# Performance work log

Hardware: AMD Instinct MI355X
Metric: run time of the kernel (lower is better)

Reference implementation:

```python
import jax, jax.numpy as jnp
import numpy as np

B, N, E = 4, 10000, 160000
F_IN, D_ATT, H = 64, 128, 8
D_K = D_ATT // H  # 16


def setup_inputs() -> dict:
    key = jax.random.key(0)
    ks = jax.random.split(key, 8)
    x = jax.random.normal(ks[0], (B, N, F_IN), dtype=jnp.float32)
    edge = jax.random.randint(ks[1], (2, E), 0, N, dtype=jnp.int64)
    scale = 0.05
    Qw = jax.random.normal(ks[2], (D_ATT, F_IN), dtype=jnp.float32) * scale
    Qb = jnp.zeros((D_ATT,), dtype=jnp.float32)
    Kw = jax.random.normal(ks[3], (D_ATT, F_IN), dtype=jnp.float32) * scale
    Kb = jnp.zeros((D_ATT,), dtype=jnp.float32)
    Vw = jax.random.normal(ks[4], (D_ATT, F_IN), dtype=jnp.float32) * scale
    Vb = jnp.zeros((D_ATT,), dtype=jnp.float32)
    return {"x": x, "Qw": Qw, "Qb": Qb, "Kw": Kw, "Kb": Kb, "Vw": Vw, "Vb": Vb, "edge": edge}


def _proj(x, W, b):
    # x: (B, N, F_IN) -> (B, N, D_K, H)  (view to (B,N,H,D_K) then transpose(2,3))
    y = jnp.einsum('bnf,af->bna', x, W) + b  # (B, N, D_ATT)
    y = y.reshape(y.shape[0], y.shape[1], H, D_K)
    return jnp.swapaxes(y, 2, 3)  # (B, N, D_K, H)


def reference(x, Qw, Qb, Kw, Kb, Vw, Vb, edge):
    q = _proj(x, Qw, Qb)  # (B, N, D_K, H)
    k = _proj(x, Kw, Kb)
    v = _proj(x, Vw, Vb)
    src = q[:, edge[0], :, :]    # (B, E, D_K, H) gather by source node
    dst_k = k[:, edge[1], :, :]  # (B, E, D_K, H) gather by dest node
    prods = jnp.sum(src * dst_k, axis=2) / np.float32(np.sqrt(D_K))  # (B, E, H)
    attention = jax.nn.softmax(prods, axis=1)  # softmax over the edge dimension, as in original
    return attention, v
```

## Files before the change

kernel.cpp:

```cpp
#include <hip/hip_runtime.h>
#include <hip/hip_bf16.h>

constexpr int B  = 4;
constexpr int N  = 10000;
constexpr int E  = 160000;
constexpr int F  = 64;
constexpr int DA = 128;
constexpr int H  = 8;
constexpr int DK = 16;
constexpr int TOTAL = B * N;

constexpr int EPB  = 256;
constexpr int NBLK = E / EPB;
constexpr int RB   = 64;

typedef __attribute__((ext_vector_type(8))) short short8v;
typedef __attribute__((ext_vector_type(4))) float f32x4;
typedef __attribute__((ext_vector_type(2))) float f32x2;

__device__ __forceinline__ unsigned pack_bf16(float a, float b) {
    unsigned ua = __builtin_bit_cast(unsigned, a);
    unsigned ub = __builtin_bit_cast(unsigned, b);
    ua = (ua + 0x7fffu + ((ua >> 16) & 1u)) >> 16;
    ub = (ub + 0x7fffu + ((ub >> 16) & 1u)) >> 16;
    return ua | (ub << 16);
}
__device__ __forceinline__ short8v cvt8(float4 a, float4 b) {
    union { unsigned u[4]; short8v s; } r;
    r.u[0] = pack_bf16(a.x, a.y);
    r.u[1] = pack_bf16(a.z, a.w);
    r.u[2] = pack_bf16(b.x, b.y);
    r.u[3] = pack_bf16(b.z, b.w);
    return r.s;
}
__device__ __forceinline__ int dot8(unsigned a, unsigned b, int c) {
#if __has_builtin(__builtin_amdgcn_sdot8)
    return __builtin_amdgcn_sdot8((int)a, (int)b, c, false);
#else
    #pragma unroll
    for (int n = 0; n < 8; ++n) {
        int av = ((int)(a << (28 - 4 * n))) >> 28;
        int bv = ((int)(b << (28 - 4 * n))) >> 28;
        c += av * bv;
    }
    return c;
#endif
}

__global__ __launch_bounds__(256) void proj_mfma(
    const float* __restrict__ x,
    const float* __restrict__ Qw, const float* __restrict__ Kw,
    const float* __restrict__ Vw,
    const float* __restrict__ Qb, const float* __restrict__ Kb,
    const float* __restrict__ Vb,
    unsigned char* __restrict__ qws, unsigned char* __restrict__ kws,
    float* __restrict__ vout)
{
    __shared__ unsigned char wlds[DA * F * 2];
    __shared__ unsigned char xlds[64 * 256];

    const int t = threadIdx.x;
    const int w = t >> 6, lane = t & 63;
    const int tn = lane & 15, g = lane >> 4;
    const int m0t = blockIdx.x * 64 + w * 16;
    const int mat = blockIdx.y;

    const float* W    = (mat == 0) ? Qw : (mat == 1) ? Kw : Vw;
    const float* bias = (mat == 0) ? Qb : (mat == 1) ? Kb : Vb;
    const float sc = (mat < 2) ? 4.0f : 1.0f;

    float bv[8];
    if (mat < 2) {
        const int base = (tn >> 1) * 16 + (tn & 1) * 8;
        #pragma unroll
        for (int a0t = 0; a0t < 8; ++a0t) bv[a0t] = bias[base + a0t] * 4.0f;
    } else {
        #pragma unroll
        for (int a0t = 0; a0t < 8; ++a0t) bv[a0t] = bias[a0t * 16 + tn];
    }

    {
        const char* xblk = (const char*)(x + (size_t)blockIdx.x * 64 * F);
        #pragma unroll
        for (int j = 0; j < 4; ++j) {
            const int A = j * 4096 + t * 16;
            float4 v = *(const float4*)(xblk + A);
            *(float4*)(xlds + (A ^ (((A >> 8) & 7) << 4))) = v;
        }
    }

    #pragma unroll
    for (int j = 0; j < 4; ++j) {
        const int A = j * 4096 + t * 16;
        const int rho = A >> 7;
        const int srow = (mat < 2)
            ? (((rho >> 1) & 7) * 16 + (rho & 1) * 8 + (rho >> 4))
            : rho;
        const float4* s4 = (const float4*)(W + srow * 64 + ((A & 127) >> 1));
        float4 v0 = s4[0], v1 = s4[1];
        uint4 v;
        v.x = pack_bf16(v0.x * sc, v0.y * sc);
        v.y = pack_bf16(v0.z * sc, v0.w * sc);
        v.z = pack_bf16(v1.x * sc, v1.y * sc);
        v.w = pack_bf16(v1.z * sc, v1.w * sc);
        *(uint4*)(wlds + (A ^ (((A >> 7) & 7) << 4))) = v;
    }
    __syncthreads();

    const int xrow = w * 16 + tn;
    const int xsw  = (xrow & 7) << 4;
    const int xb   = xrow * 256;
    const float4 x0 = *(const float4*)(xlds + ((xb + g * 32)       ^ xsw));
    const float4 x1 = *(const float4*)(xlds + ((xb + g * 32 + 16)  ^ xsw));
    const float4 x2 = *(const float4*)(xlds + ((xb + 128 + g * 32) ^ xsw));
    const float4 x3 = *(const float4*)(xlds + ((xb + 144 + g * 32) ^ xsw));
    const short8v a0 = cvt8(x0, x1);
    const short8v a1 = cvt8(x2, x3);

    const int sw = (tn & 7) << 4;

    f32x4 acc[8];
    #pragma unroll
    for (int a0t = 0; a0t < 8; ++a0t) {
        acc[a0t][0] = bv[a0t]; acc[a0t][1] = bv[a0t];
        acc[a0t][2] = bv[a0t]; acc[a0t][3] = bv[a0t];
    }
    #pragma unroll
    for (int a0t = 0; a0t < 8; ++a0t) {
        const int rowb = (a0t * 16 + tn) * 128;
        short8v b0 = *(const short8v*)(wlds + ((rowb + g * 16) ^ sw));
        short8v b1 = *(const short8v*)(wlds + ((rowb + 64 + g * 16) ^ sw));
        acc[a0t] = __builtin_amdgcn_mfma_f32_16x16x32_bf16(a0, b0, acc[a0t], 0, 0, 0);
        acc[a0t] = __builtin_amdgcn_mfma_f32_16x16x32_bf16(a1, b1, acc[a0t], 0, 0, 0);
    }

    if (mat < 2) {
        unsigned char* qk_dst = (mat == 0) ? qws : kws;
        #pragma unroll
        for (int r = 0; r < 4; ++r) {
            const int node = m0t + g * 4 + r;
            unsigned nib = 0;
            #pragma unroll
            for (int p = 0; p < 8; ++p) {
                float cl = fminf(fmaxf(acc[p][r], -7.f), 7.f);
                int iv = (int)rintf(cl);
                nib |= ((unsigned)(iv & 0xF)) << (4 * p);
            }
            *(unsigned*)(qk_dst + (size_t)node * RB + tn * 4) = nib;
        }
    } else {
        #pragma unroll
        for (int r = 0; r < 4; ++r) {
            const int node = m0t + g * 4 + r;
            float* vb = vout + (size_t)node * DA + tn * 8;
            *(float4*)vb       = make_float4(acc[0][r], acc[1][r], acc[2][r], acc[3][r]);
            *(float4*)(vb + 4) = make_float4(acc[4][r], acc[5][r], acc[6][r], acc[7][r]);
        }
    }
}

__global__ __launch_bounds__(256) void gather_dot_sm(
    const unsigned char* __restrict__ qws, const unsigned char* __restrict__ kws,
    const int* __restrict__ edge, unsigned short* __restrict__ expws,
    float* __restrict__ psum)
{
    const int b   = blockIdx.x;
    const int blk = blockIdx.y;
    const int t = threadIdx.x;
    const int w = t >> 6, lane = t & 63;
    const int g = lane >> 2, i = lane & 3;

    const unsigned char* qb = qws + (size_t)b * N * RB;
    const unsigned char* kb = kws + (size_t)b * N * RB;
    unsigned short* expb = expws + (size_t)b * E * 4;

    const int ew0 = blk * EPB + w * 64;

    const int i0 = ew0 + lane;
    const int s0p = edge[i0];
    const int d0p = edge[E + i0];

    float sa0 = 0.f, sa1 = 0.f;

    #pragma unroll
    for (int r = 0; r < 4; ++r) {
        const int el = ew0 + r * 16 + g;
        const int srcl = r * 16 + g;
        const int s = __shfl(s0p, srcl);
        const int d = __shfl(d0p, srcl);
        const uint4 q = *((const uint4*)(qb + (size_t)s * RB) + i);
        const uint4 k = *((const uint4*)(kb + (size_t)d * RB) + i);

        int dh0 = dot8(q.x, k.x, 0);  dh0 = dot8(q.y, k.y, dh0);
        int dh1 = dot8(q.z, k.z, 0);  dh1 = dot8(q.w, k.w, dh1);

        const float e0 = __expf((float)dh0 * 0.015625f);
        const float e1 = __expf((float)dh1 * 0.015625f);
        const unsigned pk = (unsigned)__builtin_amdgcn_cvt_pk_fp8_f32(e0, e1, 0, false);
        expb[(size_t)el * 4 + i] = (unsigned short)pk;
        sa0 += e0;
        sa1 += e1;
    }

    #pragma unroll
    for (int off = 4; off <= 32; off <<= 1) {
        sa0 += __shfl_xor(sa0, off);
        sa1 += __shfl_xor(sa1, off);
    }

    __shared__ float2 red[4][4];
    if (g == 0) red[w][i] = make_float2(sa0, sa1);
    __syncthreads();
    if (t < 4) {
        float s0f = 0.f, s1f = 0.f;
        #pragma unroll
        for (int ww = 0; ww < 4; ++ww) {
            float2 v = red[ww][t];
            s0f += v.x;
            s1f += v.y;
        }
        psum[((size_t)b * H + 2 * t)     * NBLK + blk] = s0f;
        psum[((size_t)b * H + 2 * t + 1) * NBLK + blk] = s1f;
    }
}

__global__ __launch_bounds__(256) void softmax_norm(
    const unsigned short* __restrict__ expws, float* __restrict__ att,
    const float* __restrict__ psum)
{
    const int b   = blockIdx.x;
    const int blk = blockIdx.y;
    const int t = threadIdx.x;
    const int w = t >> 6, lane = t & 63;

    __shared__ float inv[H];
    {
        const float* p0 = psum + ((size_t)b * H + 2 * w) * NBLK;
        const float* p1 = psum + ((size_t)b * H + 2 * w + 1) * NBLK;
        float s0 = 0.f, s1 = 0.f;
        for (int c = lane; c < NBLK; c += 64) {
            s0 += p0[c];
            s1 += p1[c];
        }
        #pragma unroll
        for (int off = 1; off < 64; off <<= 1) {
            s0 += __shfl_xor(s0, off);
            s1 += __shfl_xor(s1, off);
        }
        if (lane == 0) {
            inv[2 * w]     = 1.0f / s0;
            inv[2 * w + 1] = 1.0f / s1;
        }
    }
    __syncthreads();

    const int el = blk * EPB + t;
    const uint2 u = ((const uint2*)(expws + (size_t)b * E * 4))[el];
    float* p = att + ((size_t)b * E + el) * H;
    const f32x2 e01 = __builtin_amdgcn_cvt_pk_f32_fp8((int)u.x, false);
    const f32x2 e23 = __builtin_amdgcn_cvt_pk_f32_fp8((int)u.x, true);
    const f32x2 e45 = __builtin_amdgcn_cvt_pk_f32_fp8((int)u.y, false);
    const f32x2 e67 = __builtin_amdgcn_cvt_pk_f32_fp8((int)u.y, true);
    float4 v0, v1;
    v0.x = e01[0] * inv[0];  v0.y = e01[1] * inv[1];
    v0.z = e23[0] * inv[2];  v0.w = e23[1] * inv[3];
    v1.x = e45[0] * inv[4];  v1.y = e45[1] * inv[5];
    v1.z = e67[0] * inv[6];  v1.w = e67[1] * inv[7];
    *(float4*)p       = v0;
    *(float4*)(p + 4) = v1;
}

extern "C" void kernel_launch(void* const* d_in, const int* in_sizes, int n_in,
                              void* d_out, int out_size, void* d_ws, size_t ws_size,
                              hipStream_t stream)
{
    const float* x  = (const float*)d_in[0];
    const float* Qw = (const float*)d_in[1];
    const float* Qb = (const float*)d_in[2];
    const float* Kw = (const float*)d_in[3];
    const float* Kb = (const float*)d_in[4];
    const float* Vw = (const float*)d_in[5];
    const float* Vb = (const float*)d_in[6];
    const int*   edge = (const int*)d_in[7];

    float* out  = (float*)d_out;
    float* att  = out;
    float* vout = out + (size_t)B * E * H;

    char* w = (char*)d_ws;
    unsigned char* qws = (unsigned char*)w;
    unsigned char* kws = qws + (size_t)B * N * RB;
    unsigned short* expws = (unsigned short*)(w + 2 * (size_t)B * N * RB);
    float* psum = (float*)(expws + (size_t)B * E * 4);

    hipLaunchKernelGGL(proj_mfma, dim3(TOTAL / 64, 3), dim3(256), 0, stream,
                       x, Qw, Kw, Vw, Qb, Kb, Vb, qws, kws, vout);
    hipLaunchKernelGGL(gather_dot_sm, dim3(B, NBLK), dim3(256), 0, stream,
                       qws, kws, edge, expws, psum);
    hipLaunchKernelGGL(softmax_norm, dim3(B, NBLK), dim3(256), 0, stream,
                       expws, att, psum);
}
```

Baseline: 39.23 us.

## Fuse Q/K/V projections into one block per row tile, stage V stores via LDS

The projection kernel now computes Q, K and V for the same 64-node tile in one block instead of using a third grid dimension. The x tile is loaded and converted once and reused across all three weight matrices held in a larger LDS buffer. The V output is staged through swizzled LDS so each block writes its 32KB contiguously with coalesced float4 stores. The cost is three times the weight LDS footprint and weight conversion per block, which lowers occupancy and reduces grid parallelism.

```diff
diff --git a/kernel.cpp b/kernel.cpp
--- a/kernel.cpp
+++ b/kernel.cpp
@@ -56,27 +56,23 @@
     unsigned char* __restrict__ qws, unsigned char* __restrict__ kws,
     float* __restrict__ vout)
 {
-    __shared__ unsigned char wlds[DA * F * 2];
+    __shared__ unsigned char wlds[3 * DA * F * 2];
     __shared__ unsigned char xlds[64 * 256];
 
     const int t = threadIdx.x;
     const int w = t >> 6, lane = t & 63;
     const int tn = lane & 15, g = lane >> 4;
     const int m0t = blockIdx.x * 64 + w * 16;
-    const int mat = blockIdx.y;
-
-    const float* W    = (mat == 0) ? Qw : (mat == 1) ? Kw : Vw;
-    const float* bias = (mat == 0) ? Qb : (mat == 1) ? Kb : Vb;
-    const float sc = (mat < 2) ? 4.0f : 1.0f;
-
-    float bv[8];
-    if (mat < 2) {
+
+    float bvq[8], bvk[8], bvv[8];
+    {
         const int base = (tn >> 1) * 16 + (tn & 1) * 8;
         #pragma unroll
-        for (int a0t = 0; a0t < 8; ++a0t) bv[a0t] = bias[base + a0t] * 4.0f;
-    } else {
-        #pragma unroll
-        for (int a0t = 0; a0t < 8; ++a0t) bv[a0t] = bias[a0t * 16 + tn];
+        for (int a0t = 0; a0t < 8; ++a0t) {
+            bvq[a0t] = Qb[base + a0t] * 4.0f;
+            bvk[a0t] = Kb[base + a0t] * 4.0f;
+            bvv[a0t] = Vb[a0t * 16 + tn];
+        }
     }
 
     {
@@ -90,13 +86,16 @@
     }
 
     #pragma unroll
-    for (int j = 0; j < 4; ++j) {
-        const int A = j * 4096 + t * 16;
-        const int rho = A >> 7;
-        const int srow = (mat < 2)
+    for (int j = 0; j < 12; ++j) {
+        const float* W = (j < 4) ? Qw : (j < 8) ? Kw : Vw;
+        const float sc = (j < 8) ? 4.0f : 1.0f;
+        const int A  = j * 4096 + t * 16;
+        const int Al = A & 16383;
+        const int rho = Al >> 7;
+        const int srow = (j < 8)
             ? (((rho >> 1) & 7) * 16 + (rho & 1) * 8 + (rho >> 4))
             : rho;
-        const float4* s4 = (const float4*)(W + srow * 64 + ((A & 127) >> 1));
+        const float4* s4 = (const float4*)(W + srow * 64 + ((Al & 127) >> 1));
         float4 v0 = s4[0], v1 = s4[1];
         uint4 v;
         v.x = pack_bf16(v0.x * sc, v0.y * sc);
@@ -119,22 +118,24 @@
 
     const int sw = (tn & 7) << 4;
 
-    f32x4 acc[8];
-    #pragma unroll
-    for (int a0t = 0; a0t < 8; ++a0t) {
-        acc[a0t][0] = bv[a0t]; acc[a0t][1] = bv[a0t];
-        acc[a0t][2] = bv[a0t]; acc[a0t][3] = bv[a0t];
-    }
-    #pragma unroll
-    for (int a0t = 0; a0t < 8; ++a0t) {
-        const int rowb = (a0t * 16 + tn) * 128;
-        short8v b0 = *(const short8v*)(wlds + ((rowb + g * 16) ^ sw));
-        short8v b1 = *(const short8v*)(wlds + ((rowb + 64 + g * 16) ^ sw));
-        acc[a0t] = __builtin_amdgcn_mfma_f32_16x16x32_bf16(a0, b0, acc[a0t], 0, 0, 0);
-        acc[a0t] = __builtin_amdgcn_mfma_f32_16x16x32_bf16(a1, b1, acc[a0t], 0, 0, 0);
-    }
-
-    if (mat < 2) {
+    #pragma unroll
+    for (int mat = 0; mat < 2; ++mat) {
+        const float* bv = (mat == 0) ? bvq : bvk;
+        const unsigned char* wm = wlds + mat * (DA * F * 2);
+        f32x4 acc[8];
+        #pragma unroll
+        for (int a0t = 0; a0t < 8; ++a0t) {
+            acc[a0t][0] = bv[a0t]; acc[a0t][1] = bv[a0t];
+            acc[a0t][2] = bv[a0t]; acc[a0t][3] = bv[a0t];
+        }
+        #pragma unroll
+        for (int a0t = 0; a0t < 8; ++a0t) {
+            const int rowb = (a0t * 16 + tn) * 128;
+            short8v b0 = *(const short8v*)(wm + ((rowb + g * 16) ^ sw));
+            short8v b1 = *(const short8v*)(wm + ((rowb + 64 + g * 16) ^ sw));
+            acc[a0t] = __builtin_amdgcn_mfma_f32_16x16x32_bf16(a0, b0, acc[a0t], 0, 0, 0);
+            acc[a0t] = __builtin_amdgcn_mfma_f32_16x16x32_bf16(a1, b1, acc[a0t], 0, 0, 0);
+        }
         unsigned char* qk_dst = (mat == 0) ? qws : kws;
         #pragma unroll
         for (int r = 0; r < 4; ++r) {
@@ -148,13 +149,44 @@
             }
             *(unsigned*)(qk_dst + (size_t)node * RB + tn * 4) = nib;
         }
-    } else {
+    }
+
+    {
+        const unsigned char* wm = wlds + 2 * (DA * F * 2);
+        f32x4 acc[8];
+        #pragma unroll
+        for (int a0t = 0; a0t < 8; ++a0t) {
+            acc[a0t][0] = bvv[a0t]; acc[a0t][1] = bvv[a0t];
+            acc[a0t][2] = bvv[a0t]; acc[a0t][3] = bvv[a0t];
+        }
+        #pragma unroll
+        for (int a0t = 0; a0t < 8; ++a0t) {
+            const int rowb = (a0t * 16 + tn) * 128;
+            short8v b0 = *(const short8v*)(wm + ((rowb + g * 16) ^ sw));
+            short8v b1 = *(const short8v*)(wm + ((rowb + 64 + g * 16) ^ sw));
+            acc[a0t] = __builtin_amdgcn_mfma_f32_16x16x32_bf16(a0, b0, acc[a0t], 0, 0, 0);
+            acc[a0t] = __builtin_amdgcn_mfma_f32_16x16x32_bf16(a1, b1, acc[a0t], 0, 0, 0);
+        }
+
+        __syncthreads();
         #pragma unroll
         for (int r = 0; r < 4; ++r) {
-            const int node = m0t + g * 4 + r;
-            float* vb = vout + (size_t)node * DA + tn * 8;
-            *(float4*)vb       = make_float4(acc[0][r], acc[1][r], acc[2][r], acc[3][r]);
-            *(float4*)(vb + 4) = make_float4(acc[4][r], acc[5][r], acc[6][r], acc[7][r]);
+            const int nl = w * 16 + g * 4 + r;
+            const int base = nl * 512 + tn * 32;
+            const int vsw = (nl & 7) << 4;
+            *(float4*)(wlds + ((base) ^ vsw)) =
+                make_float4(acc[0][r], acc[1][r], acc[2][r], acc[3][r]);
+            *(float4*)(wlds + ((base + 16) ^ vsw)) =
+                make_float4(acc[4][r], acc[5][r], acc[6][r], acc[7][r]);
+        }
+        __syncthreads();
+        char* vdst = (char*)vout + (size_t)blockIdx.x * 32768;
+        #pragma unroll
+        for (int i = 0; i < 8; ++i) {
+            const int A2 = i * 4096 + t * 16;
+            const int vsw = ((A2 >> 9) & 7) << 4;
+            float4 v = *(const float4*)(wlds + (A2 ^ vsw));
+            *(float4*)(vdst + A2) = v;
         }
     }
 }
@@ -293,7 +325,7 @@
     unsigned short* expws = (unsigned short*)(w + 2 * (size_t)B * N * RB);
     float* psum = (float*)(expws + (size_t)B * E * 4);
 
-    hipLaunchKernelGGL(proj_mfma, dim3(TOTAL / 64, 3), dim3(256), 0, stream,
+    hipLaunchKernelGGL(proj_mfma, dim3(TOTAL / 64), dim3(256), 0, stream,
                        x, Qw, Kw, Vw, Qb, Kb, Vb, qws, kws, vout);
     hipLaunchKernelGGL(gather_dot_sm, dim3(B, NBLK), dim3(256), 0, stream,
                        qws, kws, edge, expws, psum);
```

Result: no change. 38.74 us (-1.2%).
